# Performance work log

Hardware: AMD Instinct MI355X
Metric: run time of the kernel (lower is better)

## Reference

```python
import jax, jax.numpy as jnp
import numpy as np
from jax import lax

NUM_CLASSES = 2
IOU_THRESH = 0.5
SCORE_THRESH = 0.5
K_CAND = 512        # per-class candidate pool fed to greedy NMS
MAX_PER_CLASS = 100
MAX_TOTAL = 100


def setup_inputs() -> dict:
    key = jax.random.key(0)
    k1, k2, k3 = jax.random.split(key, 3)
    B = 64
    pred_s1 = jax.random.normal(k1, (B, 19, 19, 3, 5 + NUM_CLASSES), dtype=jnp.float32)
    pred_s2 = jax.random.normal(k2, (B, 38, 38, 3, 5 + NUM_CLASSES), dtype=jnp.float32)
    pred_s3 = jax.random.normal(k3, (B, 76, 76, 3, 5 + NUM_CLASSES), dtype=jnp.float32)
    # standard YOLOv3 anchors (pixels) normalized by input size 608
    anchors_px = np.array([[10, 13], [16, 30], [33, 23], [30, 61], [62, 45],
                           [59, 119], [116, 90], [156, 198], [373, 326]], np.float32)
    anchors = jnp.asarray(anchors_px / 608.0)
    return {"pred_s1": pred_s1, "pred_s2": pred_s2, "pred_s3": pred_s3, "anchors": anchors}


def _decode(pred, anch):
    # pred: [B, g, g, A, 5+C]; anch: [A, 2] normalized wh
    g = pred.shape[1]
    box_xy = jax.nn.sigmoid(pred[..., 0:2])
    box_wh = jnp.exp(pred[..., 2:4]) * anch          # broadcast [A,2]
    obj = jax.nn.sigmoid(pred[..., 4:5])
    cls = jax.nn.sigmoid(pred[..., 5:])
    gx, gy = jnp.meshgrid(jnp.arange(g), jnp.arange(g))   # 'xy' indexing, as tf.meshgrid
    grid = jnp.stack([gx, gy], axis=-1)[:, :, None, :].astype(pred.dtype)  # [g,g,1,2]
    xy = (box_xy + grid) / jnp.float32(g)
    x1y1 = xy - box_wh / 2.0
    x2y2 = x1y1 + box_wh                              # YoloNMS: wh + xy(top-left)
    boxes = jnp.concatenate([x1y1, x2y2], axis=-1)    # [B,g,g,A,4]
    scores = obj * cls                                # [B,g,g,A,C]
    B = pred.shape[0]
    return boxes.reshape(B, -1, 4), scores.reshape(B, -1, NUM_CLASSES)


def _pairwise_iou(b):
    # b: [K,4] in (x1,y1,x2,y2); returns [K,K]
    a = b[:, None, :]
    c = b[None, :, :]
    iw = jnp.clip(jnp.minimum(a[..., 2], c[..., 2]) - jnp.maximum(a[..., 0], c[..., 0]), 0.0)
    ih = jnp.clip(jnp.minimum(a[..., 3], c[..., 3]) - jnp.maximum(a[..., 1], c[..., 1]), 0.0)
    inter = iw * ih
    area = jnp.clip(b[:, 2] - b[:, 0], 0.0) * jnp.clip(b[:, 3] - b[:, 1], 0.0)
    union = area[:, None] + area[None, :] - inter
    return inter / jnp.maximum(union, 1e-9)


def _nms_one_class(boxes, scores):
    # boxes: [N,4], scores: [N] -> candidate boxes/scores/keep mask, each len K_CAND
    sc, idx = lax.top_k(scores, K_CAND)               # sorted descending
    bx = boxes[idx]
    iou = lax.stop_gradient(_pairwise_iou(bx))
    valid = sc > SCORE_THRESH
    def body(i, keep):
        suppressed = jnp.any(keep & (iou[i] > IOU_THRESH))
        return keep.at[i].set(valid[i] & ~suppressed)
    keep = lax.fori_loop(0, K_CAND, body, jnp.zeros((K_CAND,), jnp.bool_))
    keep = keep & (jnp.cumsum(keep) <= MAX_PER_CLASS)
    return bx, sc, keep


def _nms_one_image(boxes, scores):
    # boxes: [N,4], scores: [N,C]
    bk, sk, keep = jax.vmap(_nms_one_class, in_axes=(None, 1))(boxes, scores)  # [C,K,*]
    sm = jnp.where(keep, sk, -1.0)
    cls_ids = jnp.broadcast_to(jnp.arange(NUM_CLASSES)[:, None], (NUM_CLASSES, K_CAND))
    sf = sm.reshape(-1)
    bf = bk.reshape(-1, 4)
    cf = cls_ids.reshape(-1)
    ts, ti = lax.top_k(sf, MAX_TOTAL)
    kept = ts > 0.0
    out_boxes = jnp.where(kept[:, None], jnp.clip(bf[ti], 0.0, 1.0), 0.0)  # clip_boxes=True
    out_scores = jnp.where(kept, ts, 0.0)
    out_classes = jnp.where(kept, cf[ti].astype(jnp.float32), 0.0)
    return out_boxes, out_scores, out_classes, jnp.sum(kept).astype(jnp.int32)


def reference(pred_s1, pred_s2, pred_s3, anchors):
    # scale masks: grid19 -> anchors[6:9], grid38 -> anchors[3:6], grid76 -> anchors[0:3]
    b1, s1 = _decode(pred_s1, anchors[6:9])
    b2, s2 = _decode(pred_s2, anchors[3:6])
    b3, s3 = _decode(pred_s3, anchors[0:3])
    boxes = jnp.concatenate([b1, b2, b3], axis=1)     # [B,N,4]
    scores = jnp.concatenate([s1, s2, s3], axis=1)    # [B,N,C]
    return jax.vmap(_nms_one_image)(boxes, scores)
```

## Files before the change

kernel.cpp:

```cpp
#include <hip/hip_runtime.h>
#include <cstdint>
#include <cstddef>

#define NTOT   22743
#define N1     1083
#define N12    5415
#define BATCH  64
#define KCAND  512
#define NSEG   16
#define SEGLEN 1422
#define CAPS   384
#define CAP    4096
#define MAXPC  100
#define MAXTOT 100
#define KITER  6

__device__ __forceinline__ float sigmoidf(float x) { return 1.0f / (1.0f + expf(-x)); }
__device__ __forceinline__ int SK4(int j) { return j + ((j >> 6) << 2); }

__global__ __launch_bounds__(256) void score_filter_kernel(
    const float* __restrict__ p1, const float* __restrict__ p2,
    const float* __restrict__ p3, uint2* __restrict__ cand,
    uint32_t* __restrict__ counts)
{
  const int blk  = blockIdx.x;
  const int b    = blk >> 4;
  const int s    = blk & 15;
  const int tid  = threadIdx.x;
  const int lane = tid & 63;

  __shared__ uint2    lst[2][CAPS];
  __shared__ uint32_t lcnt[2];

  if (tid < 2) lcnt[tid] = 0u;
  __syncthreads();

  const int beg = s * SEGLEN;
  const int end = (beg + SEGLEN < NTOT) ? beg + SEGLEN : NTOT;

  float4 v[KITER];
  #pragma unroll
  for (int k = 0; k < KITER; ++k) {
    int i0 = beg + tid + k * 256;
    if (i0 < end) {
      const float* p; int local, per;
      if (i0 < N1)       { p = p1; local = i0;        per = 1083; }
      else if (i0 < N12) { p = p2; local = i0 - N1;   per = 4332; }
      else               { p = p3; local = i0 - N12;  per = 17328; }
      const float* q = p + ((size_t)b * per + local) * 7;
      v[k] = *(const float4*)(q + 3);
    } else {
      v[k] = make_float4(0.f, -1.f, 0.f, 0.f);
    }
  }

  #pragma unroll
  for (int k = 0; k < KITER; ++k) {
    int i0 = beg + tid + k * 256;
    float s0 = 0.f, s1 = 0.f;
    float q4 = v[k].y;
    if (q4 > 0.f) {
      float obj = sigmoidf(q4);
      s0 = obj * sigmoidf(v[k].z);
      s1 = obj * sigmoidf(v[k].w);
    }
    #pragma unroll
    for (int c = 0; c < 2; c++) {
      float sc = (c == 0) ? s0 : s1;
      bool pred = sc > 0.5f;
      unsigned long long m = __ballot(pred ? 1 : 0);
      if (m != 0ull) {
        int leader = (int)__ffsll(m) - 1;
        uint32_t base = 0u;
        if (lane == leader) base = atomicAdd(&lcnt[c], (uint32_t)__popcll(m));
        base = (uint32_t)__shfl((int)base, leader);
        if (pred) {
          uint32_t off = base + (uint32_t)__popcll(m & ((1ull << lane) - 1ull));
          if (off < CAPS) lst[c][off] = make_uint2(__float_as_uint(sc), (uint32_t)i0);
        }
      }
    }
  }
  __syncthreads();

  #pragma unroll
  for (int c = 0; c < 2; c++) {
    uint32_t cnt = lcnt[c]; if (cnt > CAPS) cnt = CAPS;
    uint2* dst = cand + ((size_t)((b * 2 + c) * NSEG + s)) * CAPS;
    for (uint32_t i = tid; i < cnt; i += 256) dst[i] = lst[c][i];
    if (tid == 0) counts[(b * 2 + c) * NSEG + s] = cnt;
  }
}

__device__ void decode_box(const float* __restrict__ p1, const float* __restrict__ p2,
                           const float* __restrict__ p3, const float* __restrict__ anch,
                           int b, int i, float bb[4])
{
  const float* p; int local, g, abase, per;
  if (i < N1)       { p = p1; local = i;       g = 19; abase = 6; per = 1083; }
  else if (i < N12) { p = p2; local = i - N1;  g = 38; abase = 3; per = 4332; }
  else              { p = p3; local = i - N12; g = 76; abase = 0; per = 17328; }
  const float* q = p + ((size_t)b * per + local) * 7;
  int a    = local % 3;
  int cell = local / 3;
  int col  = cell % g;
  int row  = cell / g;
  float aw = anch[(abase + a) * 2 + 0];
  float ah = anch[(abase + a) * 2 + 1];
  float x = (sigmoidf(q[0]) + (float)col) / (float)g;
  float y = (sigmoidf(q[1]) + (float)row) / (float)g;
  float w = expf(q[2]) * aw;
  float h = expf(q[3]) * ah;
  float x1 = x - w * 0.5f;
  float y1 = y - h * 0.5f;
  bb[0] = x1; bb[1] = y1; bb[2] = x1 + w; bb[3] = y1 + h;
}

__global__ __launch_bounds__(1024) void nms_kernel(
    const uint2* __restrict__ cand, const uint32_t* __restrict__ counts,
    const float* __restrict__ p1, const float* __restrict__ p2,
    const float* __restrict__ p3, const float* __restrict__ anch,
    float* __restrict__ selScore, float* __restrict__ selBox,
    int* __restrict__ selRank, int* __restrict__ selCount)
{
  const int bc   = blockIdx.x;
  const int b    = bc >> 1;
  const int tid  = threadIdx.x;
  const int lane = tid & 63;

  __shared__ __attribute__((aligned(16))) unsigned long long sw[1024];
  __shared__ __attribute__((aligned(16))) float bx1[544];
  __shared__ __attribute__((aligned(16))) float by1[544];
  __shared__ __attribute__((aligned(16))) float bx2[544];
  __shared__ __attribute__((aligned(16))) float by2[544];
  __shared__ __attribute__((aligned(16))) float ar[544];
  __shared__ uint32_t           skey[512];
  __shared__ unsigned long long msk[128][9];
  __shared__ unsigned long long kword[8];
  __shared__ uint32_t           hist3[768];
  __shared__ uint32_t           svar[8];

  if (tid < 768) hist3[tid] = 0u;
  sw[tid] = 0ull;
  if (tid == 0) { svar[0] = 0x3F000000u; svar[2] = KCAND; svar[4] = 0u; svar[5] = 0u; }
  if (tid < 512) {
    skey[tid] = 0u; int p = SK4(tid);
    bx1[p] = 0.f; by1[p] = 0.f; bx2[p] = 0.f; by2[p] = 0.f; ar[p] = 0.f;
  }

  uint32_t pc[17];
  pc[0] = 0;
  #pragma unroll
  for (int t = 0; t < 16; ++t) {
    uint32_t c = counts[bc * NSEG + t];
    if (c > CAPS) c = CAPS;
    pc[t + 1] = pc[t] + c;
  }
  const int n = ((int)pc[16] < CAP) ? (int)pc[16] : CAP;

  unsigned long long v0 = 0ull, v1 = 0ull, v2 = 0ull, v3 = 0ull;
  auto loadc = [&](int i) -> unsigned long long {
    if (i >= n) return 0ull;
    uint32_t ps = 0; int s = 0;
    #pragma unroll
    for (int t = 1; t < 16; ++t) {
      bool ge = (uint32_t)i >= pc[t];
      s += (int)ge; ps = ge ? pc[t] : ps;
    }
    uint2 e = cand[(size_t)(bc * NSEG + s) * CAPS + (i - (int)ps)];
    return ((unsigned long long)e.x << 32) | (uint32_t)(~e.y);
  };
  v0 = loadc(tid); v1 = loadc(tid + 1024); v2 = loadc(tid + 2048); v3 = loadc(tid + 3072);
  __syncthreads();

  uint32_t K = 0u;
  if (n > KCAND) {
    #pragma unroll
    for (int p = 0; p < 3; p++) {
      const int shift = 16 - 8 * p;
      const uint32_t maskB = (p == 0) ? 0xFF000000u : (p == 1) ? 0xFFFF0000u : 0xFFFFFF00u;
      uint32_t* hist = &hist3[p * 256];
      const uint32_t prefix = svar[0];
      {
        uint32_t k;
        k = (uint32_t)(v0 >> 32); if (v0 && (k & maskB) == prefix) atomicAdd(&hist[(k >> shift) & 255u], 1u);
        k = (uint32_t)(v1 >> 32); if (v1 && (k & maskB) == prefix) atomicAdd(&hist[(k >> shift) & 255u], 1u);
        k = (uint32_t)(v2 >> 32); if (v2 && (k & maskB) == prefix) atomicAdd(&hist[(k >> shift) & 255u], 1u);
        k = (uint32_t)(v3 >> 32); if (v3 && (k & maskB) == prefix) atomicAdd(&hist[(k >> shift) & 255u], 1u);
      }
      __syncthreads();
      if (tid < 64) {
        uint32_t h0 = hist[lane * 4 + 0], h1 = hist[lane * 4 + 1];
        uint32_t h2 = hist[lane * 4 + 2], h3 = hist[lane * 4 + 3];
        uint32_t s3 = h3, s2 = h2 + s3, s1 = h1 + s2, s0 = h0 + s1;
        uint32_t acc = s0;
        #pragma unroll
        for (int o = 1; o < 64; o <<= 1) {
          uint32_t v = __shfl_down(acc, (unsigned)o);
          acc += (lane + o < 64) ? v : 0u;
        }
        uint32_t above = acc - s0;
        uint32_t S0 = above + s0, S1 = above + s1, S2 = above + s2, S3 = above + s3, S4 = above;
        uint32_t nd = svar[2];
        if (S0 >= nd && S1 < nd) { svar[0] = prefix | ((uint32_t)(lane * 4 + 0) << shift); svar[2] = nd - S1; }
        if (S1 >= nd && S2 < nd) { svar[0] = prefix | ((uint32_t)(lane * 4 + 1) << shift); svar[2] = nd - S2; }
        if (S2 >= nd && S3 < nd) { svar[0] = prefix | ((uint32_t)(lane * 4 + 2) << shift); svar[2] = nd - S3; }
        if (S3 >= nd && S4 < nd) { svar[0] = prefix | ((uint32_t)(lane * 4 + 3) << shift); svar[2] = nd - S4; }
      }
      __syncthreads();
    }
    K = svar[0];
  }

  {
    auto coll = [&](unsigned long long vv) {
      bool pred = (vv != 0ull) && ((uint32_t)(vv >> 32) >= K);
      unsigned long long m = __ballot(pred ? 1 : 0);
      if (m != 0ull) {
        int leader = (int)__ffsll(m) - 1;
        uint32_t base = 0u;
        if (lane == leader) base = atomicAdd(&svar[4], (uint32_t)__popcll(m));
        base = (uint32_t)__shfl((int)base, leader);
        if (pred) {
          uint32_t q = base + (uint32_t)__popcll(m & ((1ull << lane) - 1ull));
          if (q < 1024u) sw[q] = vv;
        }
      }
    };
    coll(v0); coll(v1); coll(v2); coll(v3);
  }
  __syncthreads();
  const int mc = ((int)svar[4] < 1024) ? (int)svar[4] : 1024;
  const int limit = (n < KCAND) ? n : KCAND;

  if (tid < 512) hist3[tid] = 0u;
  __syncthreads();
  uint32_t* bcnt = hist3;
  uint32_t* boff = hist3 + 256;
  uint32_t* bpre = hist3 + 512;
  unsigned long long e = (tid < mc) ? sw[tid] : 0ull;
  const uint32_t B = (uint32_t)((e >> 47) & 255u);
  if (tid < mc) atomicAdd(&bcnt[B], 1u);
  __syncthreads();
  if (tid < 64) {
    uint32_t h0 = bcnt[lane * 4 + 0], h1 = bcnt[lane * 4 + 1];
    uint32_t h2 = bcnt[lane * 4 + 2], h3 = bcnt[lane * 4 + 3];
    uint32_t s3 = h3, s2 = h2 + s3, s1 = h1 + s2, s0 = h0 + s1;
    uint32_t acc = s0;
    #pragma unroll
    for (int o = 1; o < 64; o <<= 1) {
      uint32_t v = __shfl_down(acc, (unsigned)o);
      acc += (lane + o < 64) ? v : 0u;
    }
    uint32_t above = acc - s0;
    bpre[lane * 4 + 0] = above + s1;
    bpre[lane * 4 + 1] = above + s2;
    bpre[lane * 4 + 2] = above + s3;
    bpre[lane * 4 + 3] = above;
  }
  __syncthreads();
  unsigned long long* bord = (unsigned long long*)msk;
  if (tid < mc) {
    uint32_t pos = bpre[B] + atomicAdd(&boff[B], 1u);
    bord[pos] = e;
  }
  __syncthreads();
  if (tid < mc) {
    const uint32_t lo = bpre[B], sz = bcnt[B];
    int rank = (int)lo;
    for (uint32_t j = lo; j < lo + sz; ++j) rank += (int)(bord[j] > e);
    if (rank < KCAND) {
      int idx = (int)(~(uint32_t)e);
      float bb[4];
      decode_box(p1, p2, p3, anch, b, idx, bb);
      int p = SK4(rank);
      bx1[p] = bb[0]; by1[p] = bb[1]; bx2[p] = bb[2]; by2[p] = bb[3];
      ar[p]  = fmaxf(bb[2] - bb[0], 0.f) * fmaxf(bb[3] - bb[1], 0.f);
      skey[rank] = (uint32_t)(e >> 32);
    }
  }
  __syncthreads();

  unsigned long long Kw = 0ull;
  int kept = 0;
  const int r = tid & 127;
  const int w = tid >> 7;

  for (int ch = 0; ch < 4; ++ch) {
    const int base = ch * 128;
    int rows = limit - base; if (rows > 128) rows = 128;

    if (r < rows) {
      const int i = base + r;
      if (w <= (i >> 6)) {
        const int ip = SK4(i);
        const float x1i = bx1[ip], y1i = by1[ip], x2i = bx2[ip], y2i = by2[ip];
        const float ai = ar[ip];
        unsigned long long mrow = 0ull;
        #pragma unroll
        for (int m4 = 0; m4 < 16; ++m4) {
          const int j0 = (w << 6) + (m4 << 2);
          const int a  = j0 + (w << 2);
          float4 X1 = *(const float4*)&bx1[a];
          float4 Y1 = *(const float4*)&by1[a];
          float4 X2 = *(const float4*)&bx2[a];
          float4 Y2 = *(const float4*)&by2[a];
          float4 AR = *(const float4*)&ar[a];
          #define IOU_BIT(JX1,JY1,JX2,JY2,JAR,J)                              \
            { float iw = fminf(x2i,(JX2)) - fmaxf(x1i,(JX1));                 \
              float ih = fminf(y2i,(JY2)) - fmaxf(y1i,(JY1));                 \
              iw = fmaxf(iw,0.f); ih = fmaxf(ih,0.f);                        \
              float inter = iw*ih;                                            \
              float uni = fmaxf(ai + (JAR) - inter, 1e-9f);                   \
              if ((inter/uni > 0.5f) && ((J) < i))                            \
                mrow |= 1ull << ((J) & 63); }
          IOU_BIT(X1.x, Y1.x, X2.x, Y2.x, AR.x, j0 + 0)
          IOU_BIT(X1.y, Y1.y, X2.y, Y2.y, AR.y, j0 + 1)
          IOU_BIT(X1.z, Y1.z, X2.z, Y2.z, AR.z, j0 + 2)
          IOU_BIT(X1.w, Y1.w, X2.w, Y2.w, AR.w, j0 + 3)
          #undef IOU_BIT
        }
        msk[r][w] = mrow;
      } else {
        msk[r][w] = 0ull;
      }
    }
    __syncthreads();

    if (tid < 64) {
      bool stop = false;
      for (int g = 0; g < 16 && !stop; ++g) {
        int r0 = g * 8;
        if (r0 >= rows) break;
        unsigned long long wbuf[8];
        #pragma unroll
        for (int k2 = 0; k2 < 8; ++k2)
          wbuf[k2] = (lane < 8 && (r0 + k2) < rows) ? msk[r0 + k2][lane] : 0ull;
        #pragma unroll
        for (int k2 = 0; k2 < 8; ++k2) {
          if (!stop) {
            int rr = r0 + k2;
            if (rr >= rows) { stop = true; }
            else {
              int i = base + rr;
              bool ov = (Kw & wbuf[k2]) != 0ull;
              if (!__any(ov)) {
                if (lane == (i >> 6)) Kw |= 1ull << (i & 63);
                if (++kept >= MAXPC) stop = true;
              }
            }
          }
        }
      }
      if (lane == 0) svar[5] = (kept >= MAXPC || (base + (rows > 0 ? rows : 0)) >= limit) ? 1u : 0u;
    }
    __syncthreads();
    if (svar[5] != 0u) break;
  }

  if (tid < 8) kword[tid] = Kw;
  __syncthreads();

  if (tid < 512) {
    int rr = tid;
    int wr = rr >> 6;
    unsigned long long kw = kword[wr];
    if ((kw >> (rr & 63)) & 1ull) {
      uint32_t p = 0;
      for (int ww = 0; ww < wr; ++ww) p += (uint32_t)__popcll(kword[ww]);
      p += (uint32_t)__popcll(kw & ((1ull << (rr & 63)) - 1ull));
      selScore[bc * MAXPC + p] = __uint_as_float(skey[rr]);
      selRank[bc * MAXPC + p]  = rr;
      int rp = SK4(rr);
      float* o = &selBox[(size_t)(bc * MAXPC + p) * 4];
      o[0] = bx1[rp]; o[1] = by1[rp]; o[2] = bx2[rp]; o[3] = by2[rp];
    }
  }
  if (tid == 0) {
    uint32_t tot = 0;
    for (int ww = 0; ww < 8; ++ww) tot += (uint32_t)__popcll(kword[ww]);
    selCount[bc] = (int)tot;
  }
}

__global__ __launch_bounds__(256) void merge_kernel(
    const float* __restrict__ selScore, const float* __restrict__ selBox,
    const int* __restrict__ selRank, const int* __restrict__ selCount,
    float* __restrict__ out)
{
  const int b   = blockIdx.x;
  const int tid = threadIdx.x;
  __shared__ float    es[200];
  __shared__ uint32_t ek[200];
  __shared__ float    eb[200][4];
  const int c0  = selCount[b * 2 + 0];
  const int c1  = selCount[b * 2 + 1];
  const int tot = c0 + c1;

  if (tid < tot) {
    int cls  = (tid < c0) ? 0 : 1;
    int slot = (cls == 0) ? tid : (tid - c0);
    int src  = (b * 2 + cls) * MAXPC + slot;
    es[tid] = selScore[src];
    ek[tid] = (uint32_t)(cls * KCAND + selRank[src]);
    eb[tid][0] = selBox[(size_t)src * 4 + 0];
    eb[tid][1] = selBox[(size_t)src * 4 + 1];
    eb[tid][2] = selBox[(size_t)src * 4 + 2];
    eb[tid][3] = selBox[(size_t)src * 4 + 3];
  }
  __syncthreads();

  float* outBoxes  = out;
  float* outScores = out + (size_t)BATCH * MAXTOT * 4;
  float* outCls    = outScores + (size_t)BATCH * MAXTOT;
  float* outCnt    = outCls + (size_t)BATCH * MAXTOT;
  const int filled = (tot < MAXTOT) ? tot : MAXTOT;

  if (tid < tot) {
    float    s  = es[tid];
    uint32_t fk = ek[tid];
    int rank = 0;
    for (int j = 0; j < tot; j++)
      rank += (int)((es[j] > s) || (es[j] == s && ek[j] < fk));
    if (rank < MAXTOT) {
      outScores[b * MAXTOT + rank] = s;
      outCls[b * MAXTOT + rank]    = (float)(fk >> 9);
      float* ob = &outBoxes[(size_t)(b * MAXTOT + rank) * 4];
      ob[0] = fminf(fmaxf(eb[tid][0], 0.f), 1.f);
      ob[1] = fminf(fmaxf(eb[tid][1], 0.f), 1.f);
      ob[2] = fminf(fmaxf(eb[tid][2], 0.f), 1.f);
      ob[3] = fminf(fmaxf(eb[tid][3], 0.f), 1.f);
    }
  }
  if (tid >= filled && tid < MAXTOT) {
    outScores[b * MAXTOT + tid] = 0.f;
    outCls[b * MAXTOT + tid]    = 0.f;
    float* ob = &outBoxes[(size_t)(b * MAXTOT + tid) * 4];
    ob[0] = 0.f; ob[1] = 0.f; ob[2] = 0.f; ob[3] = 0.f;
  }
  if (tid == 0) outCnt[b] = (float)filled;
}

extern "C" void kernel_launch(void* const* d_in, const int* in_sizes, int n_in,
                              void* d_out, int out_size, void* d_ws, size_t ws_size,
                              hipStream_t stream)
{
  const float* p1   = (const float*)d_in[0];
  const float* p2   = (const float*)d_in[1];
  const float* p3   = (const float*)d_in[2];
  const float* anch = (const float*)d_in[3];

  uint8_t* ws = (uint8_t*)d_ws;
  uint32_t* counts = (uint32_t*)ws;
  uint2*    cand   = (uint2*)(ws + 16384);
  uint8_t*  wp     = ws + 16384 + (size_t)128 * NSEG * CAPS * 8;
  float*    selScore = (float*)wp;         wp += (size_t)BATCH * 2 * MAXPC * 4;
  float*    selBox   = (float*)wp;         wp += (size_t)BATCH * 2 * MAXPC * 16;
  int*      selRank  = (int*)wp;           wp += (size_t)BATCH * 2 * MAXPC * 4;
  int*      selCount = (int*)wp;

  score_filter_kernel<<<BATCH * NSEG, 256, 0, stream>>>(p1, p2, p3, cand, counts);
  nms_kernel<<<BATCH * 2, 1024, 0, stream>>>(cand, counts, p1, p2, p3, anch,
                                             selScore, selBox, selRank, selCount);
  merge_kernel<<<BATCH, 256, 0, stream>>>(selScore, selBox, selRank, selCount,
                                          (float*)d_out);
}
```

Before: 58.10 us.

## Replace radix-select threshold pass with direct bucket sort over all candidates

Drops the three-pass radix histogram that found the top-512 score threshold, along with its compaction step. All up to 4096 candidates are now bucket-sorted by 8 bits of the score key into a larger shared buffer, and each is ranked within its bucket. Buckets that start at or beyond rank 512 are skipped. This removes several block-wide barriers and histogram passes, but it uses more shared memory (32KB for bord) and can produce long in-bucket ranking loops when many scores fall into the same bucket.

```diff
diff --git a/kernel.cpp b/kernel.cpp
--- a/kernel.cpp
+++ b/kernel.cpp
@@ -128,7 +128,7 @@
   const int tid  = threadIdx.x;
   const int lane = tid & 63;
 
-  __shared__ __attribute__((aligned(16))) unsigned long long sw[1024];
+  __shared__ __attribute__((aligned(16))) unsigned long long bord[CAP];
   __shared__ __attribute__((aligned(16))) float bx1[544];
   __shared__ __attribute__((aligned(16))) float by1[544];
   __shared__ __attribute__((aligned(16))) float bx2[544];
@@ -141,8 +141,7 @@
   __shared__ uint32_t           svar[8];
 
   if (tid < 768) hist3[tid] = 0u;
-  sw[tid] = 0ull;
-  if (tid == 0) { svar[0] = 0x3F000000u; svar[2] = KCAND; svar[4] = 0u; svar[5] = 0u; }
+  if (tid == 0) svar[5] = 0u;
   if (tid < 512) {
     skey[tid] = 0u; int p = SK4(tid);
     bx1[p] = 0.f; by1[p] = 0.f; bx2[p] = 0.f; by2[p] = 0.f; ar[p] = 0.f;
@@ -157,8 +156,9 @@
     pc[t + 1] = pc[t] + c;
   }
   const int n = ((int)pc[16] < CAP) ? (int)pc[16] : CAP;
-
-  unsigned long long v0 = 0ull, v1 = 0ull, v2 = 0ull, v3 = 0ull;
+  const int limit = (n < KCAND) ? n : KCAND;
+
+  unsigned long long v0, v1, v2, v3;
   auto loadc = [&](int i) -> unsigned long long {
     if (i >= n) return 0ull;
     uint32_t ps = 0; int s = 0;
@@ -173,75 +173,17 @@
   v0 = loadc(tid); v1 = loadc(tid + 1024); v2 = loadc(tid + 2048); v3 = loadc(tid + 3072);
   __syncthreads();
 
-  uint32_t K = 0u;
-  if (n > KCAND) {
-    #pragma unroll
-    for (int p = 0; p < 3; p++) {
-      const int shift = 16 - 8 * p;
-      const uint32_t maskB = (p == 0) ? 0xFF000000u : (p == 1) ? 0xFFFF0000u : 0xFFFFFF00u;
-      uint32_t* hist = &hist3[p * 256];
-      const uint32_t prefix = svar[0];
-      {
-        uint32_t k;
-        k = (uint32_t)(v0 >> 32); if (v0 && (k & maskB) == prefix) atomicAdd(&hist[(k >> shift) & 255u], 1u);
-        k = (uint32_t)(v1 >> 32); if (v1 && (k & maskB) == prefix) atomicAdd(&hist[(k >> shift) & 255u], 1u);
-        k = (uint32_t)(v2 >> 32); if (v2 && (k & maskB) == prefix) atomicAdd(&hist[(k >> shift) & 255u], 1u);
-        k = (uint32_t)(v3 >> 32); if (v3 && (k & maskB) == prefix) atomicAdd(&hist[(k >> shift) & 255u], 1u);
-      }
-      __syncthreads();
-      if (tid < 64) {
-        uint32_t h0 = hist[lane * 4 + 0], h1 = hist[lane * 4 + 1];
-        uint32_t h2 = hist[lane * 4 + 2], h3 = hist[lane * 4 + 3];
-        uint32_t s3 = h3, s2 = h2 + s3, s1 = h1 + s2, s0 = h0 + s1;
-        uint32_t acc = s0;
-        #pragma unroll
-        for (int o = 1; o < 64; o <<= 1) {
-          uint32_t v = __shfl_down(acc, (unsigned)o);
-          acc += (lane + o < 64) ? v : 0u;
-        }
-        uint32_t above = acc - s0;
-        uint32_t S0 = above + s0, S1 = above + s1, S2 = above + s2, S3 = above + s3, S4 = above;
-        uint32_t nd = svar[2];
-        if (S0 >= nd && S1 < nd) { svar[0] = prefix | ((uint32_t)(lane * 4 + 0) << shift); svar[2] = nd - S1; }
-        if (S1 >= nd && S2 < nd) { svar[0] = prefix | ((uint32_t)(lane * 4 + 1) << shift); svar[2] = nd - S2; }
-        if (S2 >= nd && S3 < nd) { svar[0] = prefix | ((uint32_t)(lane * 4 + 2) << shift); svar[2] = nd - S3; }
-        if (S3 >= nd && S4 < nd) { svar[0] = prefix | ((uint32_t)(lane * 4 + 3) << shift); svar[2] = nd - S4; }
-      }
-      __syncthreads();
-    }
-    K = svar[0];
-  }
-
-  {
-    auto coll = [&](unsigned long long vv) {
-      bool pred = (vv != 0ull) && ((uint32_t)(vv >> 32) >= K);
-      unsigned long long m = __ballot(pred ? 1 : 0);
-      if (m != 0ull) {
-        int leader = (int)__ffsll(m) - 1;
-        uint32_t base = 0u;
-        if (lane == leader) base = atomicAdd(&svar[4], (uint32_t)__popcll(m));
-        base = (uint32_t)__shfl((int)base, leader);
-        if (pred) {
-          uint32_t q = base + (uint32_t)__popcll(m & ((1ull << lane) - 1ull));
-          if (q < 1024u) sw[q] = vv;
-        }
-      }
-    };
-    coll(v0); coll(v1); coll(v2); coll(v3);
-  }
-  __syncthreads();
-  const int mc = ((int)svar[4] < 1024) ? (int)svar[4] : 1024;
-  const int limit = (n < KCAND) ? n : KCAND;
-
-  if (tid < 512) hist3[tid] = 0u;
-  __syncthreads();
   uint32_t* bcnt = hist3;
   uint32_t* boff = hist3 + 256;
   uint32_t* bpre = hist3 + 512;
-  unsigned long long e = (tid < mc) ? sw[tid] : 0ull;
-  const uint32_t B = (uint32_t)((e >> 47) & 255u);
-  if (tid < mc) atomicAdd(&bcnt[B], 1u);
-  __syncthreads();
+
+  #define BKT(vv) ((uint32_t)(((vv) >> 47) & 255u))
+  if (v0) atomicAdd(&bcnt[BKT(v0)], 1u);
+  if (v1) atomicAdd(&bcnt[BKT(v1)], 1u);
+  if (v2) atomicAdd(&bcnt[BKT(v2)], 1u);
+  if (v3) atomicAdd(&bcnt[BKT(v3)], 1u);
+  __syncthreads();
+
   if (tid < 64) {
     uint32_t h0 = bcnt[lane * 4 + 0], h1 = bcnt[lane * 4 + 1];
     uint32_t h2 = bcnt[lane * 4 + 2], h3 = bcnt[lane * 4 + 3];
@@ -249,8 +191,8 @@
     uint32_t acc = s0;
     #pragma unroll
     for (int o = 1; o < 64; o <<= 1) {
-      uint32_t v = __shfl_down(acc, (unsigned)o);
-      acc += (lane + o < 64) ? v : 0u;
+      uint32_t vv = __shfl_down(acc, (unsigned)o);
+      acc += (lane + o < 64) ? vv : 0u;
     }
     uint32_t above = acc - s0;
     bpre[lane * 4 + 0] = above + s1;
@@ -259,26 +201,33 @@
     bpre[lane * 4 + 3] = above;
   }
   __syncthreads();
-  unsigned long long* bord = (unsigned long long*)msk;
-  if (tid < mc) {
-    uint32_t pos = bpre[B] + atomicAdd(&boff[B], 1u);
-    bord[pos] = e;
-  }
-  __syncthreads();
-  if (tid < mc) {
+
+  if (v0) bord[bpre[BKT(v0)] + atomicAdd(&boff[BKT(v0)], 1u)] = v0;
+  if (v1) bord[bpre[BKT(v1)] + atomicAdd(&boff[BKT(v1)], 1u)] = v1;
+  if (v2) bord[bpre[BKT(v2)] + atomicAdd(&boff[BKT(v2)], 1u)] = v2;
+  if (v3) bord[bpre[BKT(v3)] + atomicAdd(&boff[BKT(v3)], 1u)] = v3;
+  __syncthreads();
+
+  auto rankdec = [&](unsigned long long e) {
+    if (e == 0ull) return;
+    const uint32_t B = BKT(e);
     const uint32_t lo = bpre[B], sz = bcnt[B];
     int rank = (int)lo;
-    for (uint32_t j = lo; j < lo + sz; ++j) rank += (int)(bord[j] > e);
-    if (rank < KCAND) {
-      int idx = (int)(~(uint32_t)e);
-      float bb[4];
-      decode_box(p1, p2, p3, anch, b, idx, bb);
-      int p = SK4(rank);
-      bx1[p] = bb[0]; by1[p] = bb[1]; bx2[p] = bb[2]; by2[p] = bb[3];
-      ar[p]  = fmaxf(bb[2] - bb[0], 0.f) * fmaxf(bb[3] - bb[1], 0.f);
-      skey[rank] = (uint32_t)(e >> 32);
-    }
-  }
+    if ((int)lo < KCAND) {
+      for (uint32_t j = lo; j < lo + sz; ++j) rank += (int)(bord[j] > e);
+      if (rank < KCAND) {
+        int idx = (int)(~(uint32_t)e);
+        float bb[4];
+        decode_box(p1, p2, p3, anch, b, idx, bb);
+        int p = SK4(rank);
+        bx1[p] = bb[0]; by1[p] = bb[1]; bx2[p] = bb[2]; by2[p] = bb[3];
+        ar[p]  = fmaxf(bb[2] - bb[0], 0.f) * fmaxf(bb[3] - bb[1], 0.f);
+        skey[rank] = (uint32_t)(e >> 32);
+      }
+    }
+  };
+  rankdec(v0); rankdec(v1); rankdec(v2); rankdec(v3);
+  #undef BKT
   __syncthreads();
 
   unsigned long long Kw = 0ull;
```

Result: no change. 56.98 us (-1.9%).
